# Kernel optimization log

Measured on AMD Instinct MI355X. Metric: run time of the kernel, lower is better.

Reference implementation:

```python
import jax, jax.numpy as jnp
import numpy as np

V, N, D, H, C = 3, 4096, 512, 128, 5  # views, nodes, in_dim, hidden, classes
NEG = -9.0e15   # mask value from original code (-9000000000000000.0)
NEG_SLOPE = 0.25


def _leaky(x, slope):
    return jnp.where(x >= 0, x, slope * x)


def setup_inputs() -> dict:
    key = jax.random.key(0)
    ks = jax.random.split(key, 24)
    g = lambda i, shape, s=0.05: (jax.random.normal(ks[i], shape, dtype=jnp.float32) * s)
    return {
        "data": jax.random.normal(ks[0], (V, N, D), dtype=jnp.float32),
        "adj": jax.random.randint(ks[1], (V, N, N), 0, 2, dtype=jnp.int32),
        "gac_w": g(2, (V, D, H)), "gac_b": g(3, (V, H)),
        "a1": g(4, (V, H)), "a2": g(5, (V, H)),
        "mlp_w": g(6, (V, D, H)), "mlp_b": g(7, (V, H)),
        "q_w": g(8, (V, H, H)), "q_b": g(9, (V, H)),
        "k_w": g(10, (V, H, H)), "k_b": g(11, (V, H)),
        "v_w": g(12, (V, H, H)), "v_b": g(13, (V, H)),
        "fc_w": g(14, (V, H, H)), "fc_b": g(15, (V, H)),
        "conf_w": g(16, (V, H, 1)), "conf_b": g(17, (V, 1)),
        "mm_w": g(18, (V * H, C)), "mm_b": g(19, (C,)),
    }


def reference(data, adj, gac_w, gac_b, a1, a2, mlp_w, mlp_b,
              q_w, q_b, k_w, k_b, v_w, v_b, fc_w, fc_b,
              conf_w, conf_b, mm_w, mm_b):
    # --- GraphAttentionConv (per view, vectorized over v) ---
    h = jnp.einsum('vnd,vdh->vnh', data, gac_w)               # spmm(input, W)
    e1 = jnp.einsum('vnh,vh->vn', h, a1)                      # h @ a1
    e2 = jnp.einsum('vnh,vh->vn', h, a2)                      # h @ a2
    e = _leaky(e1[:, :, None] + e2[:, None, :], NEG_SLOPE)    # [V,N,N] broadcast-add
    e = jnp.where(adj > 0, e, NEG)                            # mask by dense adjacency
    att = jax.nn.softmax(e, axis=-1)                          # row softmax
    feat = jnp.einsum('vnm,vmh->vnh', att, h) + gac_b[:, None, :]
    feat = _leaky(feat, NEG_SLOPE)                            # F.leaky_relu(GAC out, 0.25)
    # residual MLP branch
    feat = feat + jnp.einsum('vnd,vdh->vnh', data, mlp_w) + mlp_b[:, None, :]

    # --- StructureGuidedFeatureEnhancement (n_heads=1): per-node HxH attention ---
    Q = jnp.einsum('vnh,vho->vno', feat, q_w) + q_b[:, None, :]
    K = jnp.einsum('vnh,vho->vno', feat, k_w) + k_b[:, None, :]
    Vv = jnp.einsum('vnh,vho->vno', feat, v_w) + v_b[:, None, :]
    scale = jnp.sqrt(jnp.asarray(H, jnp.float32))
    A = Q[:, :, :, None] * K[:, :, None, :] / scale           # [V,N,H,H] outer product
    A = jax.nn.softmax(A, axis=-1)
    agg = jnp.einsum('vnio,vno->vni', A, Vv)                  # attention @ V
    agg = jnp.einsum('vnh,vho->vno', agg, fc_w) + fc_b[:, None, :]
    feat = jax.nn.relu(agg)

    # --- TCP confidence gating ---
    conf = jnp.einsum('vnh,vho->vno', feat, conf_w) + conf_b[:, None, :]  # [V,N,1]
    feat = feat * conf

    # --- concat views along feature dim, final classifier ---
    mm = jnp.transpose(feat, (1, 0, 2)).reshape(N, V * H)     # [N, V*H]
    return mm @ mm_w + mm_b                                   # MMlogit [N, C]
```

## Files before the change

### kernel.cpp

```cpp
#include <hip/hip_runtime.h>
#include <hip/hip_bf16.h>

#define V 3
#define N 4096
#define D 512
#define H 128
#define C 5
#define KS 4
#define M2 64
#define M1 32
#define LOG2E 1.4426950408889634f

typedef short short8 __attribute__((ext_vector_type(8)));
typedef float floatx4 __attribute__((ext_vector_type(4)));
typedef int   intx4  __attribute__((ext_vector_type(4)));

__device__ __forceinline__ unsigned short f2bf(float f){
  __hip_bfloat16 h = __float2bfloat16(f);
  return *reinterpret_cast<unsigned short*>(&h);
}
__device__ __forceinline__ unsigned int pk_bf16(float a, float b){
  unsigned int ua = __float_as_uint(a), ub = __float_as_uint(b);
  ua += 0x7FFFu + ((ua >> 16) & 1u);
  ub += 0x7FFFu + ((ub >> 16) & 1u);
  return (ua >> 16) | (ub & 0xFFFF0000u);
}

__global__ __launch_bounds__(256) void k0_wt(
    const float* __restrict__ gw, const float* __restrict__ mw,
    unsigned short* __restrict__ wT)
{
  const int v = blockIdx.x, m = blockIdx.y, kc = blockIdx.z;
  const int t = threadIdx.x;
  __shared__ unsigned short tr[128*72];
  const float* src = (m ? mw : gw) + (size_t)v*D*H + (size_t)kc*64*H;
  for (int i = t; i < 64*128; i += 256){
    int kk = i >> 7, col = i & 127;
    tr[col*72 + kk] = f2bf(src[i]);
  }
  __syncthreads();
  const int col = t >> 1, half = t & 1;
  uint4* dst = (uint4*)(wT + (((size_t)m*V + v)*H + col)*D + kc*64 + half*32);
  const unsigned short* s = &tr[col*72 + half*32];
  dst[0] = *(const uint4*)(s);
  dst[1] = *(const uint4*)(s + 8);
  dst[2] = *(const uint4*)(s + 16);
  dst[3] = *(const uint4*)(s + 24);
}

__global__ __launch_bounds__(512) void k1_gemm(
    const float* __restrict__ data, const unsigned short* __restrict__ wT,
    const float* __restrict__ a1, const float* __restrict__ a2,
    unsigned short* __restrict__ hT, float* __restrict__ mlp_out,
    float* __restrict__ e1g, float* __restrict__ e2g)
{
  const int v = blockIdx.y;
  const int n0 = blockIdx.x * M1;
  const int t = threadIdx.x;
  const int w = t >> 6, l = t & 63;
  __shared__ __align__(16) unsigned short AT[2][16][64][8];
  __shared__ float epart[2][M1][4];
  unsigned short* hTile = &AT[0][0][0][0];

  {
    const int r = t >> 4, oct = t & 15;
    const float4* dp = (const float4*)(data + ((size_t)v*N + n0 + r)*D + oct*32);
    float4 f[8];
    #pragma unroll
    for (int i=0;i<8;i++) f[i] = dp[i];
    #pragma unroll
    for (int q=0;q<4;q++){
      uint4 u;
      u.x = pk_bf16(f[2*q].x,   f[2*q].y);
      u.y = pk_bf16(f[2*q].z,   f[2*q].w);
      u.z = pk_bf16(f[2*q+1].x, f[2*q+1].y);
      u.w = pk_bf16(f[2*q+1].z, f[2*q+1].w);
      *(uint4*)&AT[r>>4][oct][(r&15) + 16*q][0] = u;
    }
  }
  __syncthreads();
  const int m = w >> 2, cb = (w & 3)*32;
  const int quad = l >> 4, c16 = l & 15;
  const unsigned short* b0 = wT + (((size_t)m*V + v)*H + cb + c16)*D + quad*8;
  floatx4 acc[2][2];
  #pragma unroll
  for (int rt=0;rt<2;rt++) for (int c=0;c<2;c++) acc[rt][c] = (floatx4){0.f,0.f,0.f,0.f};
  #pragma unroll
  for (int ks=0; ks<16; ks++){
    short8 a0 = *(const short8*)&AT[0][ks][l][0];
    short8 a1f = *(const short8*)&AT[1][ks][l][0];
    short8 bb0 = *(const short8*)(b0 + ks*32);
    short8 bb1 = *(const short8*)(b0 + 16*D + ks*32);
    acc[0][0] = __builtin_amdgcn_mfma_f32_16x16x32_bf16(a0,  bb0, acc[0][0], 0,0,0);
    acc[1][0] = __builtin_amdgcn_mfma_f32_16x16x32_bf16(a1f, bb0, acc[1][0], 0,0,0);
    acc[0][1] = __builtin_amdgcn_mfma_f32_16x16x32_bf16(a0,  bb1, acc[0][1], 0,0,0);
    acc[1][1] = __builtin_amdgcn_mfma_f32_16x16x32_bf16(a1f, bb1, acc[1][1], 0,0,0);
  }
  if (m == 1){
    #pragma unroll
    for (int rt=0;rt<2;rt++)
      #pragma unroll
      for (int c=0;c<2;c++)
        #pragma unroll
        for (int reg=0;reg<4;reg++){
          const int row = rt*16 + quad*4 + reg, col = cb + c*16 + c16;
          mlp_out[((size_t)v*N + n0 + row)*H + col] = acc[rt][c][reg];
        }
  } else {
    const float a1v0 = a1[v*H + cb + c16],      a2v0 = a2[v*H + cb + c16];
    const float a1v1 = a1[v*H + cb + 16 + c16], a2v1 = a2[v*H + cb + 16 + c16];
    #pragma unroll
    for (int rt=0;rt<2;rt++)
      #pragma unroll
      for (int reg=0;reg<4;reg++){
        float p1 = acc[rt][0][reg]*a1v0 + acc[rt][1][reg]*a1v1;
        float p2 = acc[rt][0][reg]*a2v0 + acc[rt][1][reg]*a2v1;
        p1 += __shfl_xor(p1,1); p1 += __shfl_xor(p1,2);
        p1 += __shfl_xor(p1,4); p1 += __shfl_xor(p1,8);
        p2 += __shfl_xor(p2,1); p2 += __shfl_xor(p2,2);
        p2 += __shfl_xor(p2,4); p2 += __shfl_xor(p2,8);
        if (c16 == 0){
          epart[0][rt*16 + quad*4 + reg][w] = p1;
          epart[1][rt*16 + quad*4 + reg][w] = p2;
        }
      }
  }
  __syncthreads();
  if (m == 0){
    #pragma unroll
    for (int rt=0;rt<2;rt++)
      #pragma unroll
      for (int c=0;c<2;c++)
        #pragma unroll
        for (int reg=0;reg<4;reg++){
          const int row = rt*16 + quad*4 + reg, col = cb + c*16 + c16;
          hTile[col*40 + row] = f2bf(acc[rt][c][reg]);
        }
  }
  __syncthreads();
  if (t < 128){
    const unsigned short* s = &hTile[t*40];
    uint4* dst = (uint4*)(hT + ((size_t)v*H + t)*N + n0);
    dst[0] = *(const uint4*)(s);
    dst[1] = *(const uint4*)(s + 8);
    dst[2] = *(const uint4*)(s + 16);
    dst[3] = *(const uint4*)(s + 24);
  } else if (t < 128 + M1){
    const int r = t - 128;
    e1g[(size_t)v*N + n0 + r] = LOG2E*(epart[0][r][0]+epart[0][r][1]+epart[0][r][2]+epart[0][r][3]);
  } else if (t < 128 + 2*M1){
    const int r = t - 128 - M1;
    e2g[(size_t)v*N + n0 + r] = LOG2E*(epart[1][r][0]+epart[1][r][1]+epart[1][r][2]+epart[1][r][3]);
  }
}

__global__ __launch_bounds__(512, 4) void k2_attn(
    const unsigned short* __restrict__ hT, const int* __restrict__ adj,
    const float* __restrict__ e1g, const float* __restrict__ e2g,
    float* __restrict__ pacc, float* __restrict__ pdenG)
{
  const int v = blockIdx.z;
  const int ksid = blockIdx.y;
  const int n0 = blockIdx.x * M2;
  const int kbase = ksid * (N/KS);
  const int t = threadIdx.x;
  const int w = t >> 6, l = t & 63;
  __shared__ __align__(16) unsigned short Afrag[2][4][4][64][8];
  __shared__ float pden_sh[M2][4];

  const int ksl  = w & 3;
  const int quad = l >> 4;
  const int rt0  = w >> 2;
  const int row0 = rt0*16 + (l & 15);
  const int row1 = row0 + 32;
  const int koff = ksl*32 + quad*8;
  const intx4* ap0 = (const intx4*)(adj + ((size_t)v*N + n0 + row0)*N + kbase + koff);
  const intx4* ap1 = (const intx4*)(adj + ((size_t)v*N + n0 + row1)*N + kbase + koff);
  const float4* ep = (const float4*)(e2g + (size_t)v*N + kbase + koff);
  const float e1r0 = e1g[(size_t)v*N + n0 + row0];
  const float e1r1 = e1g[(size_t)v*N + n0 + row1];
  float psum0 = 0.f, psum1 = 0.f;

  const int col = w*16 + (l & 15);
  const unsigned short* bcol = hT + ((size_t)v*H + col)*N + kbase + quad*8;
  floatx4 acc[4];
  #pragma unroll
  for (int rt=0;rt<4;rt++) acc[rt] = (floatx4){0.f,0.f,0.f,0.f};

  intx4  a00 = __builtin_nontemporal_load(ap0);
  intx4  a01 = __builtin_nontemporal_load(ap0 + 1);
  intx4  a10 = __builtin_nontemporal_load(ap1);
  intx4  a11 = __builtin_nontemporal_load(ap1 + 1);
  float4 ev0 = ep[0];
  float4 ev1 = ep[1];

  const int NCH = (N/KS)/128;
  #pragma unroll 1
  for (int c = 0; c < NCH; c++){
    const int buf = c & 1;
    {
      float ev[8] = {ev0.x,ev0.y,ev0.z,ev0.w, ev1.x,ev1.y,ev1.z,ev1.w};
      int   aa[8] = {a00.x,a00.y,a00.z,a00.w, a01.x,a01.y,a01.z,a01.w};
      int   bb[8] = {a10.x,a10.y,a10.z,a10.w, a11.x,a11.y,a11.z,a11.w};
      float wa[8], wb[8];
      #pragma unroll
      for (int j=0;j<8;j++){
        float ya = e1r0 + ev[j];
        ya = fmaxf(ya, 0.25f*ya);
        float ea = exp2f(ya);
        wa[j] = (aa[j] > 0) ? ea : 0.f;
        psum0 += wa[j];
        float yb = e1r1 + ev[j];
        yb = fmaxf(yb, 0.25f*yb);
        float eb = exp2f(yb);
        wb[j] = (bb[j] > 0) ? eb : 0.f;
        psum1 += wb[j];
      }
      union { short8 s; unsigned int u[4]; } pa, pb;
      #pragma unroll
      for (int j=0;j<4;j++){
        pa.u[j] = pk_bf16(wa[2*j], wa[2*j+1]);
        pb.u[j] = pk_bf16(wb[2*j], wb[2*j+1]);
      }
      *(short8*)&Afrag[buf][rt0  ][ksl][l][0] = pa.s;
      *(short8*)&Afrag[buf][rt0+2][ksl][l][0] = pb.s;
    }
    if (c+1 < NCH){
      a00 = __builtin_nontemporal_load(ap0 + (c+1)*32);
      a01 = __builtin_nontemporal_load(ap0 + (c+1)*32 + 1);
      a10 = __builtin_nontemporal_load(ap1 + (c+1)*32);
      a11 = __builtin_nontemporal_load(ap1 + (c+1)*32 + 1);
      ev0 = ep[(c+1)*32];
      ev1 = ep[(c+1)*32 + 1];
    }
    __syncthreads();
    #pragma unroll
    for (int ks=0; ks<4; ks++){
      short8 b8 = *(const short8*)(bcol + c*128 + ks*32);
      #pragma unroll
      for (int rt=0; rt<4; rt++){
        short8 a8 = *(const short8*)&Afrag[buf][rt][ks][l][0];
        acc[rt] = __builtin_amdgcn_mfma_f32_16x16x32_bf16(a8, b8, acc[rt], 0, 0, 0);
      }
    }
    __syncthreads();
  }
  psum0 += __shfl_xor(psum0, 16);
  psum0 += __shfl_xor(psum0, 32);
  psum1 += __shfl_xor(psum1, 16);
  psum1 += __shfl_xor(psum1, 32);
  if (l < 16){
    pden_sh[row0][ksl] = psum0;
    pden_sh[row1][ksl] = psum1;
  }
  __syncthreads();
  const size_t pb = ((size_t)v*KS + ksid)*(N/M2) + blockIdx.x;
  float* pa = pacc + pb*(M2*H);
  #pragma unroll
  for (int rt=0; rt<4; rt++){
    #pragma unroll
    for (int reg=0; reg<4; reg++){
      const int row = rt*16 + quad*4 + reg;
      pa[row*H + col] = acc[rt][reg];
    }
  }
  if (t < M2){
    float den = pden_sh[t][0] + pden_sh[t][1] + pden_sh[t][2] + pden_sh[t][3];
    pdenG[pb*M2 + t] = den;
  }
}

#define TN3 8
__global__ __launch_bounds__(128) void k3_sgfe(
    const float* __restrict__ pacc, const float* __restrict__ pdenG,
    const float* __restrict__ mlp_out,
    const float* __restrict__ gac_b, const float* __restrict__ mlp_b,
    const float* __restrict__ qw, const float* __restrict__ qb,
    const float* __restrict__ kw, const float* __restrict__ kb,
    const float* __restrict__ vw, const float* __restrict__ vb,
    const float* __restrict__ fcw, const float* __restrict__ fcb,
    const float* __restrict__ confw, const float* __restrict__ confb,
    float* __restrict__ feat2)
{
  const int v = blockIdx.y;
  const int n0 = blockIdx.x * TN3;
  const int t = threadIdx.x;
  const int W = t >> 6, lane = t & 63;
  __shared__ float fsT[H][12];
  __shared__ float Qs[TN3][H];
  __shared__ float2 KVs[TN3][H];
  __shared__ float As2T[H][12];
  __shared__ float rbuf2[TN3][2];
  {
    const int bx2 = blockIdx.x >> 3;
    const int lr0 = (blockIdx.x & 7) * TN3;
    const float gbv = gac_b[v*H + t];
    const float mbv = mlp_b[v*H + t];
    #pragma unroll
    for (int r=0;r<TN3;r++){
      float num = 0.f, den = 0.f;
      #pragma unroll
      for (int ks=0;ks<KS;ks++){
        const size_t pb = ((size_t)v*KS + ks)*(N/M2) + bx2;
        num += pacc[pb*(M2*H) + (size_t)(lr0 + r)*H + t];
        den += pdenG[pb*M2 + lr0 + r];
      }
      float x = num/den + gbv;
      x = (x >= 0.f) ? x : 0.25f*x;
      x += mlp_out[((size_t)v*N + n0 + r)*H + t] + mbv;
      fsT[t][r] = x;
    }
  }
  __syncthreads();
  const float* qwp = qw + (size_t)v*H*H + t;
  const float* kwp = kw + (size_t)v*H*H + t;
  const float* vwp = vw + (size_t)v*H*H + t;
  float Qr[TN3], Kr[TN3], Vr[TN3];
  {
    const float qbv = qb[v*H+t], kbv = kb[v*H+t], vbv = vb[v*H+t];
    #pragma unroll
    for (int r=0;r<TN3;r++){ Qr[r]=qbv; Kr[r]=kbv; Vr[r]=vbv; }
  }
  for (int i=0;i<H;i++){
    float wq = qwp[(size_t)i*H];
    float wk = kwp[(size_t)i*H];
    float wv = vwp[(size_t)i*H];
    float4 f0 = *(const float4*)&fsT[i][0];
    float4 f1 = *(const float4*)&fsT[i][4];
    float fv[8] = {f0.x,f0.y,f0.z,f0.w, f1.x,f1.y,f1.z,f1.w};
    #pragma unroll
    for (int r=0;r<TN3;r++){
      Qr[r] = fmaf(fv[r], wq, Qr[r]);
      Kr[r] = fmaf(fv[r], wk, Kr[r]);
      Vr[r] = fmaf(fv[r], wv, Vr[r]);
    }
  }
  #pragma unroll
  for (int r=0;r<TN3;r++){
    Qs[r][t] = Qr[r];
    KVs[r][t] = make_float2(Kr[r], Vr[r]);
  }
  __syncthreads();
  const float invs = 0.08838834764831845f;
  #pragma unroll
  for (int p=0;p<4;p++){
    const int r = 2*p + W;
    const float qa = Qs[r][lane]   * invs;
    const float qb2 = Qs[r][lane+64] * invs;
    float sA=0.f, aA=0.f, sB=0.f, aB=0.f;
    const float4* kvp = (const float4*)&KVs[r][0];
    #pragma unroll 4
    for (int oo=0; oo<H/2; oo++){
      float4 kv2 = kvp[oo];
      float eA0 = __expf(qa*kv2.x);  sA += eA0; aA = fmaf(eA0, kv2.y, aA);
      float eA1 = __expf(qa*kv2.z);  sA += eA1; aA = fmaf(eA1, kv2.w, aA);
      float eB0 = __expf(qb2*kv2.x); sB += eB0; aB = fmaf(eB0, kv2.y, aB);
      float eB1 = __expf(qb2*kv2.z); sB += eB1; aB = fmaf(eB1, kv2.w, aB);
    }
    As2T[lane][r]    = aA/sA;
    As2T[lane+64][r] = aB/sB;
  }
  __syncthreads();
  const float* fcwp = fcw + (size_t)v*H*H + t;
  const float fcbv = fcb[v*H+t];
  float g[TN3];
  #pragma unroll
  for (int r=0;r<TN3;r++) g[r] = fcbv;
  for (int i=0;i<H;i++){
    float fw = fcwp[(size_t)i*H];
    float4 a0 = *(const float4*)&As2T[i][0];
    float4 a1v = *(const float4*)&As2T[i][4];
    g[0] = fmaf(a0.x, fw, g[0]);  g[1] = fmaf(a0.y, fw, g[1]);
    g[2] = fmaf(a0.z, fw, g[2]);  g[3] = fmaf(a0.w, fw, g[3]);
    g[4] = fmaf(a1v.x, fw, g[4]); g[5] = fmaf(a1v.y, fw, g[5]);
    g[6] = fmaf(a1v.z, fw, g[6]); g[7] = fmaf(a1v.w, fw, g[7]);
  }
  const float cwv = confw[v*H+t];
  const float cbv = confb[v];
  #pragma unroll
  for (int r=0;r<TN3;r++){
    g[r] = fmaxf(g[r], 0.f);
    float psm = g[r]*cwv;
    #pragma unroll
    for (int o=32;o>0;o>>=1) psm += __shfl_down(psm,o);
    if (lane==0) rbuf2[r][W] = psm;
  }
  __syncthreads();
  #pragma unroll
  for (int r=0;r<TN3;r++){
    const float conf = rbuf2[r][0] + rbuf2[r][1] + cbv;
    feat2[((size_t)v*N + n0 + r)*H + t] = g[r]*conf;
  }
}

__global__ __launch_bounds__(64) void k4_cls(
    const float* __restrict__ feat2,
    const float* __restrict__ mm_w, const float* __restrict__ mm_b,
    float* __restrict__ out)
{
  const int n = blockIdx.x, t = threadIdx.x;
  float a[C] = {0,0,0,0,0};
  for (int j=t; j<V*H; j+=64){
    int vv = j >> 7, hh = j & (H-1);
    float f = feat2[((size_t)vv*N + n)*H + hh];
    #pragma unroll
    for (int c=0;c<C;c++) a[c] = fmaf(f, mm_w[j*C+c], a[c]);
  }
  #pragma unroll
  for (int c=0;c<C;c++){
    #pragma unroll
    for (int o=32;o>0;o>>=1) a[c] += __shfl_down(a[c],o);
  }
  if (t==0){
    #pragma unroll
    for (int c=0;c<C;c++) out[(size_t)n*C+c] = a[c] + mm_b[c];
  }
}

extern "C" void kernel_launch(void* const* d_in, const int* in_sizes, int n_in,
                              void* d_out, int out_size, void* d_ws, size_t ws_size,
                              hipStream_t stream)
{
  (void)in_sizes; (void)n_in; (void)out_size; (void)ws_size;
  const float* data  = (const float*)d_in[0];
  const int*   adj   = (const int*)d_in[1];
  const float* gac_w = (const float*)d_in[2];
  const float* gac_b = (const float*)d_in[3];
  const float* a1    = (const float*)d_in[4];
  const float* a2    = (const float*)d_in[5];
  const float* mlp_w = (const float*)d_in[6];
  const float* mlp_b = (const float*)d_in[7];
  const float* q_w   = (const float*)d_in[8];
  const float* q_b   = (const float*)d_in[9];
  const float* k_w   = (const float*)d_in[10];
  const float* k_b   = (const float*)d_in[11];
  const float* v_w   = (const float*)d_in[12];
  const float* v_b   = (const float*)d_in[13];
  const float* fc_w  = (const float*)d_in[14];
  const float* fc_b  = (const float*)d_in[15];
  const float* cw    = (const float*)d_in[16];
  const float* cb    = (const float*)d_in[17];
  const float* mm_w  = (const float*)d_in[18];
  const float* mm_b  = (const float*)d_in[19];

  float* ws = (float*)d_ws;
  const size_t VNH = (size_t)V*N*H;
  float* mlp   = ws;
  float* feat2 = ws + VNH;
  float* e1    = ws + 2*VNH;
  float* e2    = e1 + (size_t)V*N;
  unsigned short* hT = (unsigned short*)(e2 + (size_t)V*N);
  unsigned short* wT = hT + VNH;
  float* pacc  = (float*)(wT + (size_t)2*V*H*D);
  float* pden  = pacc + (size_t)V*KS*(N/M2)*M2*H;

  k0_wt  <<<dim3(V, 2, D/64), 256, 0, stream>>>(gac_w, mlp_w, wT);
  k1_gemm<<<dim3(N/M1, V),    512, 0, stream>>>(data, wT, a1, a2, hT, mlp, e1, e2);
  k2_attn<<<dim3(N/M2, KS, V),512, 0, stream>>>(hT, adj, e1, e2, pacc, pden);
  k3_sgfe<<<dim3(N/TN3, V),   128, 0, stream>>>(pacc, pden, mlp, gac_b, mlp_b,
                                                q_w, q_b, k_w, k_b, v_w, v_b,
                                                fc_w, fc_b, cw, cb, feat2);
  k4_cls <<<dim3(N),           64, 0, stream>>>(feat2, mm_w, mm_b, (float*)d_out);
}
```

Before: 447.3 us.

## Move SGFE Q/K/V and FC projections onto bf16 MFMA with pre-transposed weights

Adds a prep kernel that converts the Q, K, V and FC weights to transposed bf16. The SGFE kernel now handles 16 nodes per 256-thread block and computes the Q/K/V and FC projections with 16x16x32 bf16 MFMA instead of scalar fp32 FMA loops. The confidence reduction is redone to match the MFMA output layout. This removes scalar FMA work and repeated fp32 weight reads, at the cost of bf16 rounding on the features, the attention output and the weights.

New measurement: 430.1 us. 3.9% less time.

```diff
diff --git a/kernel.cpp b/kernel.cpp
--- a/kernel.cpp
+++ b/kernel.cpp
@@ -41,6 +41,29 @@
   __syncthreads();
   const int col = t >> 1, half = t & 1;
   uint4* dst = (uint4*)(wT + (((size_t)m*V + v)*H + col)*D + kc*64 + half*32);
+  const unsigned short* s = &tr[col*72 + half*32];
+  dst[0] = *(const uint4*)(s);
+  dst[1] = *(const uint4*)(s + 8);
+  dst[2] = *(const uint4*)(s + 16);
+  dst[3] = *(const uint4*)(s + 24);
+}
+
+__global__ __launch_bounds__(256) void k0b_wt(
+    const float* __restrict__ qw, const float* __restrict__ kw,
+    const float* __restrict__ vw, const float* __restrict__ fw,
+    unsigned short* __restrict__ wq4T)
+{
+  const int v = blockIdx.x, m = blockIdx.y, kc = blockIdx.z;
+  const int t = threadIdx.x;
+  __shared__ unsigned short tr[128*72];
+  const float* src = (m==0?qw: m==1?kw: m==2?vw: fw) + (size_t)v*H*H + (size_t)kc*64*H;
+  for (int i = t; i < 64*128; i += 256){
+    int kk = i >> 7, col = i & 127;
+    tr[col*72 + kk] = f2bf(src[i]);
+  }
+  __syncthreads();
+  const int col = t >> 1, half = t & 1;
+  uint4* dst = (uint4*)(wq4T + (((size_t)m*V + v)*H + col)*H + kc*64 + half*32);
   const unsigned short* s = &tr[col*72 + half*32];
   dst[0] = *(const uint4*)(s);
   dst[1] = *(const uint4*)(s + 8);
@@ -270,83 +293,92 @@
   }
 }
 
-#define TN3 8
-__global__ __launch_bounds__(128) void k3_sgfe(
+__global__ __launch_bounds__(256) void k3_sgfe(
     const float* __restrict__ pacc, const float* __restrict__ pdenG,
     const float* __restrict__ mlp_out,
     const float* __restrict__ gac_b, const float* __restrict__ mlp_b,
-    const float* __restrict__ qw, const float* __restrict__ qb,
-    const float* __restrict__ kw, const float* __restrict__ kb,
-    const float* __restrict__ vw, const float* __restrict__ vb,
-    const float* __restrict__ fcw, const float* __restrict__ fcb,
+    const unsigned short* __restrict__ wq4T,
+    const float* __restrict__ qb, const float* __restrict__ kb,
+    const float* __restrict__ vb, const float* __restrict__ fcb,
     const float* __restrict__ confw, const float* __restrict__ confb,
     float* __restrict__ feat2)
 {
   const int v = blockIdx.y;
-  const int n0 = blockIdx.x * TN3;
+  const int n0 = blockIdx.x * 16;
   const int t = threadIdx.x;
-  const int W = t >> 6, lane = t & 63;
-  __shared__ float fsT[H][12];
-  __shared__ float Qs[TN3][H];
-  __shared__ float2 KVs[TN3][H];
-  __shared__ float As2T[H][12];
-  __shared__ float rbuf2[TN3][2];
+  const int w = t >> 6, l = t & 63;
+  const int c16 = l & 15, quad = l >> 4;
+  __shared__ __align__(16) unsigned short Ffrag[4][64][8];
+  __shared__ __align__(16) unsigned short Gfrag[4][64][8];
+  __shared__ float Qs[16][H];
+  __shared__ float2 KVs[16][H];
+  __shared__ float pc[16][4];
+  __shared__ float confs[16];
+
   {
-    const int bx2 = blockIdx.x >> 3;
-    const int lr0 = (blockIdx.x & 7) * TN3;
-    const float gbv = gac_b[v*H + t];
-    const float mbv = mlp_b[v*H + t];
-    #pragma unroll
-    for (int r=0;r<TN3;r++){
+    const int col = t & 127, rh = t >> 7;
+    const int bx2 = blockIdx.x >> 2;
+    const int lr0 = (blockIdx.x & 3) * 16;
+    const float gbv = gac_b[v*H + col];
+    const float mbv = mlp_b[v*H + col];
+    const int ks = col >> 5, q2 = (col & 31) >> 3, j = col & 7;
+    #pragma unroll
+    for (int i=0;i<8;i++){
+      const int r = rh*8 + i;
       float num = 0.f, den = 0.f;
       #pragma unroll
-      for (int ks=0;ks<KS;ks++){
-        const size_t pb = ((size_t)v*KS + ks)*(N/M2) + bx2;
-        num += pacc[pb*(M2*H) + (size_t)(lr0 + r)*H + t];
+      for (int s=0;s<KS;s++){
+        const size_t pb = ((size_t)v*KS + s)*(N/M2) + bx2;
+        num += pacc[pb*(M2*H) + (size_t)(lr0+r)*H + col];
         den += pdenG[pb*M2 + lr0 + r];
       }
       float x = num/den + gbv;
       x = (x >= 0.f) ? x : 0.25f*x;
-      x += mlp_out[((size_t)v*N + n0 + r)*H + t] + mbv;
-      fsT[t][r] = x;
-    }
-  }
-  __syncthreads();
-  const float* qwp = qw + (size_t)v*H*H + t;
-  const float* kwp = kw + (size_t)v*H*H + t;
-  const float* vwp = vw + (size_t)v*H*H + t;
-  float Qr[TN3], Kr[TN3], Vr[TN3];
+      x += mlp_out[((size_t)v*N + n0 + r)*H + col] + mbv;
+      Ffrag[ks][r + 16*q2][j] = f2bf(x);
+    }
+  }
+  __syncthreads();
+  const int colw0 = 2*w*16 + c16;
   {
-    const float qbv = qb[v*H+t], kbv = kb[v*H+t], vbv = vb[v*H+t];
-    #pragma unroll
-    for (int r=0;r<TN3;r++){ Qr[r]=qbv; Kr[r]=kbv; Vr[r]=vbv; }
-  }
-  for (int i=0;i<H;i++){
-    float wq = qwp[(size_t)i*H];
-    float wk = kwp[(size_t)i*H];
-    float wv = vwp[(size_t)i*H];
-    float4 f0 = *(const float4*)&fsT[i][0];
-    float4 f1 = *(const float4*)&fsT[i][4];
-    float fv[8] = {f0.x,f0.y,f0.z,f0.w, f1.x,f1.y,f1.z,f1.w};
-    #pragma unroll
-    for (int r=0;r<TN3;r++){
-      Qr[r] = fmaf(fv[r], wq, Qr[r]);
-      Kr[r] = fmaf(fv[r], wk, Kr[r]);
-      Vr[r] = fmaf(fv[r], wv, Vr[r]);
-    }
-  }
-  #pragma unroll
-  for (int r=0;r<TN3;r++){
-    Qs[r][t] = Qr[r];
-    KVs[r][t] = make_float2(Kr[r], Vr[r]);
+    const unsigned short* bq = wq4T + (((size_t)0*V + v)*H + colw0)*H + quad*8;
+    const unsigned short* bk = wq4T + (((size_t)1*V + v)*H + colw0)*H + quad*8;
+    const unsigned short* bv = wq4T + (((size_t)2*V + v)*H + colw0)*H + quad*8;
+    floatx4 aq[2], ak[2], av[2];
+    #pragma unroll
+    for (int c=0;c<2;c++){ aq[c]=(floatx4){0,0,0,0}; ak[c]=(floatx4){0,0,0,0}; av[c]=(floatx4){0,0,0,0}; }
+    #pragma unroll
+    for (int ks=0; ks<4; ks++){
+      short8 a8 = *(const short8*)&Ffrag[ks][l][0];
+      #pragma unroll
+      for (int c=0;c<2;c++){
+        short8 q8 = *(const short8*)(bq + (size_t)c*16*H + ks*32);
+        short8 k8 = *(const short8*)(bk + (size_t)c*16*H + ks*32);
+        short8 v8 = *(const short8*)(bv + (size_t)c*16*H + ks*32);
+        aq[c] = __builtin_amdgcn_mfma_f32_16x16x32_bf16(a8, q8, aq[c], 0,0,0);
+        ak[c] = __builtin_amdgcn_mfma_f32_16x16x32_bf16(a8, k8, ak[c], 0,0,0);
+        av[c] = __builtin_amdgcn_mfma_f32_16x16x32_bf16(a8, v8, av[c], 0,0,0);
+      }
+    }
+    #pragma unroll
+    for (int c=0;c<2;c++){
+      const int col = colw0 + c*16;
+      const float qbv = qb[v*H+col], kbv = kb[v*H+col], vbv = vb[v*H+col];
+      #pragma unroll
+      for (int reg=0;reg<4;reg++){
+        const int node = quad*4 + reg;
+        Qs[node][col] = aq[c][reg] + qbv;
+        KVs[node][col] = make_float2(ak[c][reg] + kbv, av[c][reg] + vbv);
+      }
+    }
   }
   __syncthreads();
   const float invs = 0.08838834764831845f;
   #pragma unroll
   for (int p=0;p<4;p++){
-    const int r = 2*p + W;
-    const float qa = Qs[r][lane]   * invs;
-    const float qb2 = Qs[r][lane+64] * invs;
+    const int r = 4*w + p;
+    const float qa  = Qs[r][l]    * invs;
+    const float qb2 = Qs[r][l+64] * invs;
     float sA=0.f, aA=0.f, sB=0.f, aB=0.f;
     const float4* kvp = (const float4*)&KVs[r][0];
     #pragma unroll 4
@@ -357,39 +389,58 @@
       float eB0 = __expf(qb2*kv2.x); sB += eB0; aB = fmaf(eB0, kv2.y, aB);
       float eB1 = __expf(qb2*kv2.z); sB += eB1; aB = fmaf(eB1, kv2.w, aB);
     }
-    As2T[lane][r]    = aA/sA;
-    As2T[lane+64][r] = aB/sB;
-  }
-  __syncthreads();
-  const float* fcwp = fcw + (size_t)v*H*H + t;
-  const float fcbv = fcb[v*H+t];
-  float g[TN3];
-  #pragma unroll
-  for (int r=0;r<TN3;r++) g[r] = fcbv;
-  for (int i=0;i<H;i++){
-    float fw = fcwp[(size_t)i*H];
-    float4 a0 = *(const float4*)&As2T[i][0];
-    float4 a1v = *(const float4*)&As2T[i][4];
-    g[0] = fmaf(a0.x, fw, g[0]);  g[1] = fmaf(a0.y, fw, g[1]);
-    g[2] = fmaf(a0.z, fw, g[2]);  g[3] = fmaf(a0.w, fw, g[3]);
-    g[4] = fmaf(a1v.x, fw, g[4]); g[5] = fmaf(a1v.y, fw, g[5]);
-    g[6] = fmaf(a1v.z, fw, g[6]); g[7] = fmaf(a1v.w, fw, g[7]);
-  }
-  const float cwv = confw[v*H+t];
-  const float cbv = confb[v];
-  #pragma unroll
-  for (int r=0;r<TN3;r++){
-    g[r] = fmaxf(g[r], 0.f);
-    float psm = g[r]*cwv;
-    #pragma unroll
-    for (int o=32;o>0;o>>=1) psm += __shfl_down(psm,o);
-    if (lane==0) rbuf2[r][W] = psm;
-  }
-  __syncthreads();
-  #pragma unroll
-  for (int r=0;r<TN3;r++){
-    const float conf = rbuf2[r][0] + rbuf2[r][1] + cbv;
-    feat2[((size_t)v*N + n0 + r)*H + t] = g[r]*conf;
+    Gfrag[l>>5][r + 16*((l&31)>>3)][l&7] = f2bf(aA/sA);
+    Gfrag[2 + (l>>5)][r + 16*((l&31)>>3)][l&7] = f2bf(aB/sB);
+  }
+  __syncthreads();
+  const unsigned short* bf = wq4T + (((size_t)3*V + v)*H + colw0)*H + quad*8;
+  floatx4 af[2];
+  af[0]=(floatx4){0,0,0,0}; af[1]=(floatx4){0,0,0,0};
+  #pragma unroll
+  for (int ks=0; ks<4; ks++){
+    short8 a8 = *(const short8*)&Gfrag[ks][l][0];
+    #pragma unroll
+    for (int c=0;c<2;c++){
+      short8 b8 = *(const short8*)(bf + (size_t)c*16*H + ks*32);
+      af[c] = __builtin_amdgcn_mfma_f32_16x16x32_bf16(a8, b8, af[c], 0,0,0);
+    }
+  }
+  float g[2][4];
+  float pn[4] = {0.f,0.f,0.f,0.f};
+  #pragma unroll
+  for (int c=0;c<2;c++){
+    const int col = colw0 + c*16;
+    const float fcbv = fcb[v*H+col];
+    const float cwv  = confw[v*H+col];
+    #pragma unroll
+    for (int reg=0;reg<4;reg++){
+      float gg = fmaxf(af[c][reg] + fcbv, 0.f);
+      g[c][reg] = gg;
+      pn[reg] += gg*cwv;
+    }
+  }
+  #pragma unroll
+  for (int reg=0;reg<4;reg++){
+    pn[reg] += __shfl_xor(pn[reg], 1);
+    pn[reg] += __shfl_xor(pn[reg], 2);
+    pn[reg] += __shfl_xor(pn[reg], 4);
+    pn[reg] += __shfl_xor(pn[reg], 8);
+  }
+  if (c16 == 0){
+    #pragma unroll
+    for (int reg=0;reg<4;reg++) pc[quad*4 + reg][w] = pn[reg];
+  }
+  __syncthreads();
+  if (t < 16) confs[t] = pc[t][0] + pc[t][1] + pc[t][2] + pc[t][3] + confb[v];
+  __syncthreads();
+  #pragma unroll
+  for (int c=0;c<2;c++){
+    const int col = colw0 + c*16;
+    #pragma unroll
+    for (int reg=0;reg<4;reg++){
+      const int node = quad*4 + reg;
+      feat2[((size_t)v*N + n0 + node)*H + col] = g[c][reg]*confs[node];
+    }
   }
 }
 
@@ -449,16 +500,18 @@
   float* feat2 = ws + VNH;
   float* e1    = ws + 2*VNH;
   float* e2    = e1 + (size_t)V*N;
-  unsigned short* hT = (unsigned short*)(e2 + (size_t)V*N);
-  unsigned short* wT = hT + VNH;
-  float* pacc  = (float*)(wT + (size_t)2*V*H*D);
+  unsigned short* hT   = (unsigned short*)(e2 + (size_t)V*N);
+  unsigned short* wT   = hT + VNH;
+  unsigned short* wq4T = wT + (size_t)2*V*H*D;
+  float* pacc  = (float*)(wq4T + (size_t)4*V*H*H);
   float* pden  = pacc + (size_t)V*KS*(N/M2)*M2*H;
 
   k0_wt  <<<dim3(V, 2, D/64), 256, 0, stream>>>(gac_w, mlp_w, wT);
+  k0b_wt <<<dim3(V, 4, H/64), 256, 0, stream>>>(q_w, k_w, v_w, fc_w, wq4T);
   k1_gemm<<<dim3(N/M1, V),    512, 0, stream>>>(data, wT, a1, a2, hT, mlp, e1, e2);
   k2_attn<<<dim3(N/M2, KS, V),512, 0, stream>>>(hT, adj, e1, e2, pacc, pden);
-  k3_sgfe<<<dim3(N/TN3, V),   128, 0, stream>>>(pacc, pden, mlp, gac_b, mlp_b,
-                                                q_w, q_b, k_w, k_b, v_w, v_b,
-                                                fc_w, fc_b, cw, cb, feat2);
+  k3_sgfe<<<dim3(N/16, V),    256, 0, stream>>>(pacc, pden, mlp, gac_b, mlp_b,
+                                                wq4T, q_b, k_b, v_b, fc_b,
+                                                cw, cb, feat2);
   k4_cls <<<dim3(N),           64, 0, stream>>>(feat2, mm_w, mm_b, (float*)d_out);
 }
```
